# Kernel optimization log

Hardware: AMD Instinct MI355X
Metric: run time of the kernel (lower is better)

The kernel has to match this reference:

```python
import jax, jax.numpy as jnp
import numpy as np

N, K, D = 32768, 8192, 64

def setup_inputs() -> dict:
    key = jax.random.key(0)
    kx, kc = jax.random.split(key)
    x = jax.random.normal(kx, (N, D), dtype=jnp.float32)
    codebook = jax.random.normal(kc, (K, D), dtype=jnp.float32)
    return {"x": x, "codebook": codebook}

def reference(x, codebook):
    # Faithful to: argmin(((codebook[None] - x[:, None])**2).sum(-1), -1)
    # Computed via the expanded squared distance to avoid the [N, K, D]
    # constant per row and does not affect argmin, but we include it so the
    # distance matrix matches the original math exactly.
    x_sq = jnp.sum(x * x, axis=-1, keepdims=True)          # [N, 1]
    c_sq = jnp.sum(codebook * codebook, axis=-1)           # [K]
    cross = jnp.einsum('nd,kd->nk', x, codebook)           # [N, K]
    dists = x_sq - 2.0 * cross + c_sq[None, :]             # [N, K]
    return jnp.argmin(dists, axis=-1)                      # [N] int32
```

## Files before the change

kernel.cpp:

```cpp
#include <hip/hip_runtime.h>
#include <math.h>


typedef __attribute__((ext_vector_type(8)))  _Float16 h8v;
typedef __attribute__((ext_vector_type(16))) float f16v;

constexpr int NROWS = 32768;
constexpr int KC    = 8192;
constexpr int DD    = 64;
constexpr int TPB   = 512;
constexpr int PTPB  = 256;
constexpr int NKB   = 16;
constexpr int RPB   = 1024;
constexpr int SROWS = 128;
constexpr int NSUB  = RPB / SROWS;
constexpr int CH    = 512;

__device__ __forceinline__ void split2h(float v, _Float16& h1, _Float16& h2) {
  const float av = fabsf(v);
  _Float16 a = (_Float16)v;
  if (av < 6.1035156e-5f) a = (_Float16)0.f;
  h1 = a;
  h2 = (_Float16)((v - (float)a) * 4096.f);
}

__device__ __forceinline__ unsigned fkey(float f) {
  const unsigned u = __float_as_uint(f);
  return u ^ (((unsigned)((int)u >> 31)) | 0x80000000u);
}

__global__ void vq_pre_kernel(const float* __restrict__ cb,
                              _Float16* __restrict__ cbSwz,
                              float* __restrict__ csq,
                              unsigned long long* __restrict__ gkey) {
  const int gidx = blockIdx.x * PTPB + threadIdx.x;
  gkey[gidx] = 0xFFFFFFFFFFFFFFFFull;
  const int code = gidx >> 2;
  const int kc4  = gidx & 3;
  const float* cp = cb + (size_t)code * DD + kc4 * 16;
  float v[16];
#pragma unroll
  for (int d = 0; d < 16; d += 4) {
    const float4 g = *(const float4*)(cp + d);
    v[d] = g.x; v[d + 1] = g.y; v[d + 2] = g.z; v[d + 3] = g.w;
  }
  float s = 0.f;
#pragma unroll
  for (int d = 0; d < 16; ++d) s = fmaf(v[d], v[d], s);
  s += __shfl_xor(s, 1, 64);
  s += __shfl_xor(s, 2, 64);
  _Float16 p1[16], p2[16];
#pragma unroll
  for (int d = 0; d < 16; ++d) split2h(v[d], p1[d], p2[d]);
  const int g = code >> 5, l = code & 31;
  _Float16* base = cbSwz + (size_t)g * 4096;
#pragma unroll
  for (int p = 0; p < 2; ++p) {
    const _Float16* pl = p ? p2 : p1;
#pragma unroll
    for (int h = 0; h < 2; ++h) {
      h8v wv;
#pragma unroll
      for (int j = 0; j < 8; ++j) wv[j] = pl[h * 8 + j];
      *(h8v*)(base + (p * 4 + kc4) * 512 + (h * 32 + l) * 8) = wv;
    }
  }
  if (kc4 == 0) csq[code] = s;
}

#define SPLITWRITE(PAR)                                                        \
  {                                                                            \
    const float ff[16] = {LR0.x, LR0.y, LR0.z, LR0.w, LR1.x, LR1.y, LR1.z,     \
                          LR1.w, LR2.x, LR2.y, LR2.z, LR2.w, LR3.x, LR3.y,     \
                          LR3.z, LR3.w};                                       \
    _Pragma("unroll")                                                          \
    for (int h = 0; h < 2; ++h) {                                              \
      h8v p1v, p2v;                                                            \
      _Pragma("unroll")                                                        \
      for (int j = 0; j < 8; ++j) {                                            \
        _Float16 a_, b_;                                                       \
        split2h(ff[h * 8 + j], a_, b_);                                        \
        p1v[j] = a_; p2v[j] = b_;                                              \
      }                                                                        \
      *(h8v*)&bufX[PAR][((sg2 * 2 + 0) * 4 + skc) * CH + (h * 32 + sr31) * 8] = p1v; \
      *(h8v*)&bufX[PAR][((sg2 * 2 + 1) * 4 + skc) * CH + (h * 32 + sr31) * 8] = p2v; \
    }                                                                          \
  }

__global__ __launch_bounds__(TPB, 2)
void vq_mfma_kernel(const float* __restrict__ x, const _Float16* __restrict__ cbSwz,
                    const float* __restrict__ csq_g,
                    unsigned long long* __restrict__ gkey) {
  __shared__ alignas(16) _Float16 bufX[2][32 * CH];
  __shared__ alignas(16) unsigned long long ldsRed[8][SROWS];

  const int tid  = threadIdx.x;
  const int lane = tid & 63;
  const int w    = tid >> 6;
  const int half = lane >> 5;
  const int col  = lane & 31;
  const int kb   = blockIdx.x & (NKB - 1);
  const int bn   = blockIdx.x >> 4;
  const size_t nbase = (size_t)bn * RPB;

  h8v cbfr[2][2][4];
#pragma unroll
  for (int q = 0; q < 2; ++q)
#pragma unroll
    for (int p = 0; p < 2; ++p)
#pragma unroll
      for (int kc = 0; kc < 4; ++kc)
        cbfr[q][p][kc] = *(const h8v*)(cbSwz +
            (size_t)(kb * 16 + w * 2 + q) * 4096 + (p * 4 + kc) * 512 + lane * 8);

  const int cbase = kb * 512 + w * 64 + 4 * half;
  float csq[2][16];
#pragma unroll
  for (int q = 0; q < 2; ++q)
#pragma unroll
    for (int i = 0; i < 16; ++i)
      csq[q][i] = csq_g[cbase + q * 32 + (i & 3) + 8 * (i >> 2)];

  const int sr = tid & 127, skc = tid >> 7;
  const int sg2 = sr >> 5, sr31 = sr & 31;

  float4 LR0, LR1, LR2, LR3;
  {
    const float* xp = x + (nbase + sr) * DD + skc * 16;
    LR0 = ((const float4*)xp)[0]; LR1 = ((const float4*)xp)[1];
    LR2 = ((const float4*)xp)[2]; LR3 = ((const float4*)xp)[3];
    SPLITWRITE(0);
  }
  asm volatile("s_waitcnt lgkmcnt(0)\n\ts_barrier" ::: "memory");

  const f16v Z = {0.f,0.f,0.f,0.f,0.f,0.f,0.f,0.f,0.f,0.f,0.f,0.f,0.f,0.f,0.f,0.f};

#pragma unroll 1
  for (int t = 0; t < NSUB; ++t) {
    const int par = t & 1;
    if (t + 1 < NSUB) {
      const float* xp = x + (nbase + (size_t)(t + 1) * SROWS + sr) * DD + skc * 16;
      LR0 = ((const float4*)xp)[0]; LR1 = ((const float4*)xp)[1];
      LR2 = ((const float4*)xp)[2]; LR3 = ((const float4*)xp)[3];
    }
#pragma unroll
    for (int cg = 0; cg < 4; ++cg) {
      h8v xfr[2][4];
#pragma unroll
      for (int p = 0; p < 2; ++p)
#pragma unroll
        for (int kc = 0; kc < 4; ++kc)
          xfr[p][kc] = *(const h8v*)&bufX[par][((cg * 2 + p) * 4 + kc) * CH + lane * 8];

      __builtin_amdgcn_s_setprio(1);
      f16v A0 = Z, B0 = Z, A1 = Z, B1 = Z;
#pragma unroll
      for (int kc = 0; kc < 4; ++kc) {
        A0 = __builtin_amdgcn_mfma_f32_32x32x16_f16(cbfr[0][0][kc], xfr[0][kc], A0, 0, 0, 0);
        A1 = __builtin_amdgcn_mfma_f32_32x32x16_f16(cbfr[1][0][kc], xfr[0][kc], A1, 0, 0, 0);
        B0 = __builtin_amdgcn_mfma_f32_32x32x16_f16(cbfr[0][0][kc], xfr[1][kc], B0, 0, 0, 0);
        B1 = __builtin_amdgcn_mfma_f32_32x32x16_f16(cbfr[1][0][kc], xfr[1][kc], B1, 0, 0, 0);
      }
#pragma unroll
      for (int kc = 0; kc < 4; ++kc) {
        B0 = __builtin_amdgcn_mfma_f32_32x32x16_f16(cbfr[0][1][kc], xfr[0][kc], B0, 0, 0, 0);
        B1 = __builtin_amdgcn_mfma_f32_32x32x16_f16(cbfr[1][1][kc], xfr[0][kc], B1, 0, 0, 0);
      }
      __builtin_amdgcn_s_setprio(0);

      float bd = INFINITY;
      unsigned bc = 0u;
#pragma unroll
      for (int i = 0; i < 16; ++i) {
        const float di = fmaf(-2.f, fmaf(B0[i], 2.44140625e-4f, A0[i]), csq[0][i]);
        if (di < bd) { bd = di; bc = (unsigned)(cbase + (i & 3) + 8 * (i >> 2)); }
      }
#pragma unroll
      for (int i = 0; i < 16; ++i) {
        const float di = fmaf(-2.f, fmaf(B1[i], 2.44140625e-4f, A1[i]), csq[1][i]);
        if (di < bd) { bd = di; bc = (unsigned)(cbase + 32 + (i & 3) + 8 * (i >> 2)); }
      }
      unsigned long long key = ((unsigned long long)fkey(bd) << 32) | bc;
      const unsigned long long o = __shfl_xor(key, 32, 64);
      if (o < key) key = o;
      if (half == 0) ldsRed[w][cg * 32 + col] = key;
    }
    if (t + 1 < NSUB) SPLITWRITE(par ^ 1);
    asm volatile("s_waitcnt lgkmcnt(0)\n\ts_barrier" ::: "memory");
    if (tid < SROWS) {
      unsigned long long k0 = ldsRed[0][tid];
#pragma unroll
      for (int w2 = 1; w2 < 8; ++w2) {
        const unsigned long long o2 = ldsRed[w2][tid];
        if (o2 < k0) k0 = o2;
      }
      atomicMin(&gkey[nbase + (size_t)t * SROWS + tid], k0);
    }
    asm volatile("s_barrier" ::: "memory");
  }
}

__global__ void vq_fin_kernel(const unsigned long long* __restrict__ gkey,
                              int* __restrict__ out) {
  const int n = blockIdx.x * PTPB + threadIdx.x;
  out[n] = (int)(unsigned)(gkey[n] & 0xFFFFFFFFull);
}

extern "C" void kernel_launch(void* const* d_in, const int* in_sizes, int n_in,
                              void* d_out, int out_size, void* d_ws, size_t ws_size,
                              hipStream_t stream) {
  const float* x  = (const float*)d_in[0];
  const float* cb = (const float*)d_in[1];
  int* out = (int*)d_out;

  _Float16* cbSwz = (_Float16*)d_ws;
  float* csq_g = (float*)((char*)d_ws + (size_t)KC * DD * 2 * 2);
  unsigned long long* gkey =
      (unsigned long long*)((char*)csq_g + (size_t)KC * 4);

  vq_pre_kernel<<<dim3(KC * 4 / PTPB), dim3(PTPB), 0, stream>>>(cb, cbSwz, csq_g, gkey);
  vq_mfma_kernel<<<dim3(NKB * (NROWS / RPB)), dim3(TPB), 0, stream>>>(
      x, cbSwz, csq_g, gkey);
  vq_fin_kernel<<<dim3(NROWS / PTPB), dim3(PTPB), 0, stream>>>(gkey, out);
}
```

Baseline: 159.6 us.

## Shrink blocks to 256 threads, double codebook split, serialize accumulator pairs

Halves the block size (4 waves), doubles the number of codebook partitions per row block, and halves the row sub-tile to 64 rows, shrinking LDS use. The MFMA accumulation is split into two sequential groups of A/B accumulators instead of four live at once, which lowers register pressure so that launch bounds can allow 3 blocks per CU. The aim is higher occupancy and better latency hiding. In exchange there are more sub-tile iterations with barriers and twice as many atomicMin updates per row, and less MFMA work in flight per wave.

```diff
diff --git a/kernel.cpp b/kernel.cpp
--- a/kernel.cpp
+++ b/kernel.cpp
@@ -8,13 +8,12 @@
 constexpr int NROWS = 32768;
 constexpr int KC    = 8192;
 constexpr int DD    = 64;
-constexpr int TPB   = 512;
+constexpr int TPB   = 256;
 constexpr int PTPB  = 256;
-constexpr int NKB   = 16;
+constexpr int NKB   = 32;
 constexpr int RPB   = 1024;
-constexpr int SROWS = 128;
+constexpr int SROWS = 64;
 constexpr int NSUB  = RPB / SROWS;
-constexpr int CH    = 512;
 
 __device__ __forceinline__ void split2h(float v, _Float16& h1, _Float16& h2) {
   const float av = fabsf(v);
@@ -82,17 +81,17 @@
         split2h(ff[h * 8 + j], a_, b_);                                        \
         p1v[j] = a_; p2v[j] = b_;                                              \
       }                                                                        \
-      *(h8v*)&bufX[PAR][((sg2 * 2 + 0) * 4 + skc) * CH + (h * 32 + sr31) * 8] = p1v; \
-      *(h8v*)&bufX[PAR][((sg2 * 2 + 1) * 4 + skc) * CH + (h * 32 + sr31) * 8] = p2v; \
+      *(h8v*)&bufX[PAR][((sg2 * 2 + 0) * 4 + skc) * 512 + (h * 32 + sr31) * 8] = p1v; \
+      *(h8v*)&bufX[PAR][((sg2 * 2 + 1) * 4 + skc) * 512 + (h * 32 + sr31) * 8] = p2v; \
     }                                                                          \
   }
 
-__global__ __launch_bounds__(TPB, 2)
+__global__ __launch_bounds__(TPB, 3)
 void vq_mfma_kernel(const float* __restrict__ x, const _Float16* __restrict__ cbSwz,
                     const float* __restrict__ csq_g,
                     unsigned long long* __restrict__ gkey) {
-  __shared__ alignas(16) _Float16 bufX[2][32 * CH];
-  __shared__ alignas(16) unsigned long long ldsRed[8][SROWS];
+  __shared__ alignas(16) _Float16 bufX[2][8192];
+  __shared__ alignas(16) unsigned long long ldsRed[4][SROWS];
 
   const int tid  = threadIdx.x;
   const int lane = tid & 63;
@@ -100,7 +99,7 @@
   const int half = lane >> 5;
   const int col  = lane & 31;
   const int kb   = blockIdx.x & (NKB - 1);
-  const int bn   = blockIdx.x >> 4;
+  const int bn   = blockIdx.x >> 5;
   const size_t nbase = (size_t)bn * RPB;
 
   h8v cbfr[2][2][4];
@@ -111,9 +110,9 @@
 #pragma unroll
       for (int kc = 0; kc < 4; ++kc)
         cbfr[q][p][kc] = *(const h8v*)(cbSwz +
-            (size_t)(kb * 16 + w * 2 + q) * 4096 + (p * 4 + kc) * 512 + lane * 8);
-
-  const int cbase = kb * 512 + w * 64 + 4 * half;
+            (size_t)(kb * 8 + w * 2 + q) * 4096 + (p * 4 + kc) * 512 + lane * 8);
+
+  const int cbase = kb * 256 + w * 64 + 4 * half;
   float csq[2][16];
 #pragma unroll
   for (int q = 0; q < 2; ++q)
@@ -121,7 +120,7 @@
     for (int i = 0; i < 16; ++i)
       csq[q][i] = csq_g[cbase + q * 32 + (i & 3) + 8 * (i >> 2)];
 
-  const int sr = tid & 127, skc = tid >> 7;
+  const int sr = lane, skc = w;
   const int sg2 = sr >> 5, sr31 = sr & 31;
 
   float4 LR0, LR1, LR2, LR3;
@@ -144,41 +143,53 @@
       LR2 = ((const float4*)xp)[2]; LR3 = ((const float4*)xp)[3];
     }
 #pragma unroll
-    for (int cg = 0; cg < 4; ++cg) {
+    for (int cg = 0; cg < 2; ++cg) {
       h8v xfr[2][4];
 #pragma unroll
       for (int p = 0; p < 2; ++p)
 #pragma unroll
         for (int kc = 0; kc < 4; ++kc)
-          xfr[p][kc] = *(const h8v*)&bufX[par][((cg * 2 + p) * 4 + kc) * CH + lane * 8];
-
-      __builtin_amdgcn_s_setprio(1);
-      f16v A0 = Z, B0 = Z, A1 = Z, B1 = Z;
-#pragma unroll
-      for (int kc = 0; kc < 4; ++kc) {
-        A0 = __builtin_amdgcn_mfma_f32_32x32x16_f16(cbfr[0][0][kc], xfr[0][kc], A0, 0, 0, 0);
-        A1 = __builtin_amdgcn_mfma_f32_32x32x16_f16(cbfr[1][0][kc], xfr[0][kc], A1, 0, 0, 0);
-        B0 = __builtin_amdgcn_mfma_f32_32x32x16_f16(cbfr[0][0][kc], xfr[1][kc], B0, 0, 0, 0);
-        B1 = __builtin_amdgcn_mfma_f32_32x32x16_f16(cbfr[1][0][kc], xfr[1][kc], B1, 0, 0, 0);
-      }
-#pragma unroll
-      for (int kc = 0; kc < 4; ++kc) {
-        B0 = __builtin_amdgcn_mfma_f32_32x32x16_f16(cbfr[0][1][kc], xfr[0][kc], B0, 0, 0, 0);
-        B1 = __builtin_amdgcn_mfma_f32_32x32x16_f16(cbfr[1][1][kc], xfr[0][kc], B1, 0, 0, 0);
-      }
-      __builtin_amdgcn_s_setprio(0);
+          xfr[p][kc] = *(const h8v*)&bufX[par][((cg * 2 + p) * 4 + kc) * 512 + lane * 8];
 
       float bd = INFINITY;
       unsigned bc = 0u;
-#pragma unroll
-      for (int i = 0; i < 16; ++i) {
-        const float di = fmaf(-2.f, fmaf(B0[i], 2.44140625e-4f, A0[i]), csq[0][i]);
-        if (di < bd) { bd = di; bc = (unsigned)(cbase + (i & 3) + 8 * (i >> 2)); }
+      {
+        __builtin_amdgcn_s_setprio(1);
+        f16v A = Z, B = Z;
+#pragma unroll
+        for (int kc = 0; kc < 4; ++kc)
+          A = __builtin_amdgcn_mfma_f32_32x32x16_f16(cbfr[0][0][kc], xfr[0][kc], A, 0, 0, 0);
+#pragma unroll
+        for (int kc = 0; kc < 4; ++kc)
+          B = __builtin_amdgcn_mfma_f32_32x32x16_f16(cbfr[0][0][kc], xfr[1][kc], B, 0, 0, 0);
+#pragma unroll
+        for (int kc = 0; kc < 4; ++kc)
+          B = __builtin_amdgcn_mfma_f32_32x32x16_f16(cbfr[0][1][kc], xfr[0][kc], B, 0, 0, 0);
+        __builtin_amdgcn_s_setprio(0);
+#pragma unroll
+        for (int i = 0; i < 16; ++i) {
+          const float di = fmaf(-2.f, fmaf(B[i], 2.44140625e-4f, A[i]), csq[0][i]);
+          if (di < bd) { bd = di; bc = (unsigned)(cbase + (i & 3) + 8 * (i >> 2)); }
+        }
       }
-#pragma unroll
-      for (int i = 0; i < 16; ++i) {
-        const float di = fmaf(-2.f, fmaf(B1[i], 2.44140625e-4f, A1[i]), csq[1][i]);
-        if (di < bd) { bd = di; bc = (unsigned)(cbase + 32 + (i & 3) + 8 * (i >> 2)); }
+      {
+        __builtin_amdgcn_s_setprio(1);
+        f16v A = Z, B = Z;
+#pragma unroll
+        for (int kc = 0; kc < 4; ++kc)
+          A = __builtin_amdgcn_mfma_f32_32x32x16_f16(cbfr[1][0][kc], xfr[0][kc], A, 0, 0, 0);
+#pragma unroll
+        for (int kc = 0; kc < 4; ++kc)
+          B = __builtin_amdgcn_mfma_f32_32x32x16_f16(cbfr[1][0][kc], xfr[1][kc], B, 0, 0, 0);
+#pragma unroll
+        for (int kc = 0; kc < 4; ++kc)
+          B = __builtin_amdgcn_mfma_f32_32x32x16_f16(cbfr[1][1][kc], xfr[0][kc], B, 0, 0, 0);
+        __builtin_amdgcn_s_setprio(0);
+#pragma unroll
+        for (int i = 0; i < 16; ++i) {
+          const float di = fmaf(-2.f, fmaf(B[i], 2.44140625e-4f, A[i]), csq[1][i]);
+          if (di < bd) { bd = di; bc = (unsigned)(cbase + 32 + (i & 3) + 8 * (i >> 2)); }
+        }
       }
       unsigned long long key = ((unsigned long long)fkey(bd) << 32) | bc;
       const unsigned long long o = __shfl_xor(key, 32, 64);
@@ -190,7 +201,7 @@
     if (tid < SROWS) {
       unsigned long long k0 = ldsRed[0][tid];
 #pragma unroll
-      for (int w2 = 1; w2 < 8; ++w2) {
+      for (int w2 = 1; w2 < 4; ++w2) {
         const unsigned long long o2 = ldsRed[w2][tid];
         if (o2 < k0) k0 = o2;
       }
```

After: 254.0 us. +59.2%, slower.
